# Performance work log

Measured on AMD Instinct MI355X. Metric: run time of the kernel, lower is better.

The kernel has to match this reference:

```python
import jax, jax.numpy as jnp
import numpy as np

N, E, D, H, K = 8192, 8, 1024, 4096, 2


def setup_inputs() -> dict:
    key = jax.random.key(0)
    ks = jax.random.split(key, 12)
    s = 0.02  # init scale for weights
    return {
        "x": jax.random.normal(ks[0], (N, D), jnp.float32),
        "noise": jax.random.normal(ks[1], (N, E), jnp.float32),
        "Wg_w": jax.random.normal(ks[2], (D, E), jnp.float32) * s,
        "Wg_b": jnp.zeros((E,), jnp.float32),
        "Wn_w": jax.random.normal(ks[3], (D, E), jnp.float32) * s,
        "Wn_b": jnp.zeros((E,), jnp.float32),
        "w1": jax.random.normal(ks[4], (E, D, H), jnp.float32) * s,
        "b1": jnp.zeros((E, H), jnp.float32),
        "w2": jax.random.normal(ks[5], (E, H, D), jnp.float32) * s,
        "b2": jnp.zeros((E, D), jnp.float32),
        "k": K,
    }


def reference(x, noise, Wg_w, Wg_b, Wn_w, Wn_b, w1, b1, w2, b2, k):
    # --- noisy top-k gating: H(x) = Wg(x) + noise * softplus(Wn(x)) ---
    g_logits = x @ Wg_w + Wg_b                       # [N, E]
    n_scale = jax.nn.softplus(x @ Wn_w + Wn_b)       # [N, E]
    h = g_logits + noise * n_scale                   # [N, E]
    topk_vals, topk_inds = jax.lax.top_k(h, k)       # [N, k]
    gates = jax.nn.softmax(topk_vals, axis=-1)       # [N, k]

    # Scatter top-k gates into a dense [N, E] map (zeros for unselected experts),
    # so the weighted combine is exactly sum_j gates[n,j] * expert_{inds[n,j]}(x_n).
    n_tok, n_exp = h.shape
    dense_gates = jnp.zeros((n_tok, n_exp), h.dtype).at[
        jnp.arange(n_tok)[:, None], topk_inds
    ].set(gates)                                     # [N, E]

    # --- per-expert 2-layer MLP: fc2(relu(fc1(x))) ---
    hid = jax.nn.relu(jnp.einsum('nd,edh->neh', x, w1) + b1)  # [N, E, H]
    y = jnp.einsum('neh,ehd->ned', hid, w2) + b2              # [N, E, D]
    out = jnp.einsum('ned,ne->nd', y, dense_gates)            # [N, D]
    return out
```

## Files before the change

### kernel.cpp

```cpp
#include <hip/hip_runtime.h>
#include <hip/hip_bf16.h>

#define NTOK 8192
#define NEXP 8
#define DMODEL 1024
#define DHID 4096

typedef __bf16 bf16x8 __attribute__((ext_vector_type(8)));
typedef float f32x4 __attribute__((ext_vector_type(4)));

__device__ __forceinline__ unsigned short f2bf(float f) {
  return __builtin_bit_cast(unsigned short, __float2bfloat16(f));
}

__device__ __forceinline__ void gload_lds16(const void* g, void* l) {
  __builtin_amdgcn_global_load_lds(
      (const __attribute__((address_space(1))) unsigned int*)g,
      (__attribute__((address_space(3))) unsigned int*)l, 16, 0, 0);
}

__device__ __forceinline__ int imin(int a, int b) { return a < b ? a : b; }

constexpr size_t OFF_XB   = 0;
constexpr size_t OFF_W1T  = OFF_XB + (size_t)NTOK * DMODEL * 2;
constexpr size_t OFF_W2T  = OFF_W1T + (size_t)NEXP * DHID * DMODEL * 2;
constexpr size_t OFF_HID  = OFF_W2T + (size_t)NEXP * DMODEL * DHID * 2;
constexpr size_t OFF_IDX  = OFF_HID + (size_t)NTOK * 2 * DHID * 2;
constexpr size_t OFF_GATE = OFF_IDX + (size_t)NTOK * 2 * 4;
constexpr size_t OFF_LIST = OFF_GATE + (size_t)NTOK * 2 * 4;
constexpr size_t OFF_CNT  = OFF_LIST + (size_t)NTOK * 2 * 4;
constexpr size_t OFF_OFFS = OFF_CNT + 128;
constexpr size_t OFF_CUR  = OFF_OFFS + 128;

__global__ __launch_bounds__(256) void prep_kernel(
    const float* __restrict__ w1, unsigned short* __restrict__ w1t,
    const float* __restrict__ x, const float* __restrict__ noise,
    const float* __restrict__ Wg_w, const float* __restrict__ Wg_b,
    const float* __restrict__ Wn_w, const float* __restrict__ Wn_b,
    unsigned short* __restrict__ xb, int* __restrict__ topk_idx,
    float* __restrict__ topk_gate, int* __restrict__ counts) {
  __shared__ float sh[64][65];
  const int bid = blockIdx.x;

  if (bid < 8192) {
    int e = bid >> 10, rem = bid & 1023;
    const int R = DMODEL, C = DHID;
    const float* in = w1 + (size_t)e * R * C;
    unsigned short* outp = w1t + (size_t)e * R * C;
    int r0 = (rem >> 6) * 64;
    int c0 = (rem & 63) * 64;
    int tx = threadIdx.x & 15, ty = threadIdx.x >> 4;
#pragma unroll
    for (int p = 0; p < 4; ++p) {
      int row = ty + p * 16;
      float4 v = *(const float4*)&in[(size_t)(r0 + row) * C + c0 + tx * 4];
      sh[row][tx * 4 + 0] = v.x;
      sh[row][tx * 4 + 1] = v.y;
      sh[row][tx * 4 + 2] = v.z;
      sh[row][tx * 4 + 3] = v.w;
    }
    __syncthreads();
#pragma unroll
    for (int p = 0; p < 4; ++p) {
      int crow = ty + p * 16;
      ushort4 o;
      o.x = f2bf(sh[tx * 4 + 0][crow]);
      o.y = f2bf(sh[tx * 4 + 1][crow]);
      o.z = f2bf(sh[tx * 4 + 2][crow]);
      o.w = f2bf(sh[tx * 4 + 3][crow]);
      *(ushort4*)&outp[(size_t)(c0 + crow) * R + r0 + tx * 4] = o;
    }
    return;
  }

  int g = bid - 8192;
  int wave = threadIdx.x >> 6;
  int lane = threadIdx.x & 63;
  int n = g * 4 + wave;
  if (n >= NTOK) return;

  float ag[8] = {0.f, 0.f, 0.f, 0.f, 0.f, 0.f, 0.f, 0.f};
  float an[8] = {0.f, 0.f, 0.f, 0.f, 0.f, 0.f, 0.f, 0.f};
  const float* xr = x + (size_t)n * DMODEL;
  unsigned short* xbr = xb + (size_t)n * DMODEL;
#pragma unroll 4
  for (int i = 0; i < DMODEL / 64; ++i) {
    int d = lane + i * 64;
    float xv = xr[d];
    xbr[d] = f2bf(xv);
    const float4* wg = (const float4*)(Wg_w + (size_t)d * 8);
    const float4* wn = (const float4*)(Wn_w + (size_t)d * 8);
    float4 g0 = wg[0], g1 = wg[1];
    float4 n0 = wn[0], n1 = wn[1];
    ag[0] += xv * g0.x; ag[1] += xv * g0.y; ag[2] += xv * g0.z; ag[3] += xv * g0.w;
    ag[4] += xv * g1.x; ag[5] += xv * g1.y; ag[6] += xv * g1.z; ag[7] += xv * g1.w;
    an[0] += xv * n0.x; an[1] += xv * n0.y; an[2] += xv * n0.z; an[3] += xv * n0.w;
    an[4] += xv * n1.x; an[5] += xv * n1.y; an[6] += xv * n1.z; an[7] += xv * n1.w;
  }
#pragma unroll
  for (int off = 32; off > 0; off >>= 1) {
#pragma unroll
    for (int j = 0; j < 8; ++j) {
      ag[j] += __shfl_down(ag[j], off, 64);
      an[j] += __shfl_down(an[j], off, 64);
    }
  }
  if (lane == 0) {
    float h[8];
#pragma unroll
    for (int e = 0; e < 8; ++e) {
      float gl = ag[e] + Wg_b[e];
      float z = an[e] + Wn_b[e];
      float sp = fmaxf(z, 0.f) + log1pf(expf(-fabsf(z)));
      h[e] = gl + noise[(size_t)n * 8 + e] * sp;
    }
    int i0 = 0; float v0 = h[0];
#pragma unroll
    for (int e = 1; e < 8; ++e)
      if (h[e] > v0) { v0 = h[e]; i0 = e; }
    int i1 = -1; float v1 = -1e30f;
#pragma unroll
    for (int e = 0; e < 8; ++e)
      if (e != i0 && h[e] > v1) { v1 = h[e]; i1 = e; }
    float e1 = expf(v1 - v0);
    float inv = 1.f / (1.f + e1);
    topk_idx[n * 2] = i0;
    topk_idx[n * 2 + 1] = i1;
    topk_gate[n * 2] = inv;
    topk_gate[n * 2 + 1] = e1 * inv;
    atomicAdd(&counts[i0], 1);
    atomicAdd(&counts[i1], 1);
  }
}

__global__ void scan_kernel(const int* __restrict__ counts,
                            int* __restrict__ offsets, int* __restrict__ cursor) {
  if (threadIdx.x == 0) {
    int acc = 0;
    for (int e = 0; e < NEXP; ++e) {
      offsets[e] = acc;
      cursor[e] = acc;
      acc += counts[e];
    }
    offsets[NEXP] = acc;
  }
}

__global__ void scatter_kernel(const int* __restrict__ topk_idx,
                               int* __restrict__ cursor, int* __restrict__ list) {
  int n = blockIdx.x * 256 + threadIdx.x;
  if (n >= NTOK) return;
#pragma unroll
  for (int j = 0; j < 2; ++j) {
    int e = topk_idx[n * 2 + j];
    int pos = atomicAdd(&cursor[e], 1);
    list[pos] = n * 2 + j;
  }
}

#define VMW(N) asm volatile("s_waitcnt vmcnt(" #N ")" ::: "memory")

template <int MODE>
__global__ __launch_bounds__(256, 4) void expert_gemm(
    const unsigned short* __restrict__ Asrc, const unsigned short* __restrict__ Bt,
    const float* __restrict__ bias, const int* __restrict__ offsets,
    const int* __restrict__ list, const float* __restrict__ gates,
    unsigned short* __restrict__ hid, float* __restrict__ out,
    const float* __restrict__ w2src, unsigned short* __restrict__ w2dst) {
  constexpr int Krow = MODE ? DHID : DMODEL;
  constexpr int Nout = MODE ? DMODEL : DHID;
  constexpr int NT = Krow / 32;

  __shared__ alignas(16) unsigned short Al[3][128 * 32];
  __shared__ alignas(16) unsigned short Bl[3][128 * 32];

  const int gx = gridDim.x, gy = gridDim.y;
  const int lin = blockIdx.x + gx * (blockIdx.y + gy * blockIdx.z);

  if (MODE == 0 && lin >= 16384) {
    float (*sh)[65] = reinterpret_cast<float(*)[65]>(&Al[0][0]);
    int t = lin - 16384;
    int e = t >> 10, rem = t & 1023;
    const int R = DHID, C = DMODEL;
    const float* in = w2src + (size_t)e * R * C;
    unsigned short* outp = w2dst + (size_t)e * R * C;
    int r0 = (rem >> 4) * 64;
    int c0 = (rem & 15) * 64;
    int tx = threadIdx.x & 15, ty = threadIdx.x >> 4;
#pragma unroll
    for (int p = 0; p < 4; ++p) {
      int row = ty + p * 16;
      float4 v = *(const float4*)&in[(size_t)(r0 + row) * C + c0 + tx * 4];
      sh[row][tx * 4 + 0] = v.x;
      sh[row][tx * 4 + 1] = v.y;
      sh[row][tx * 4 + 2] = v.z;
      sh[row][tx * 4 + 3] = v.w;
    }
    __syncthreads();
#pragma unroll
    for (int p = 0; p < 4; ++p) {
      int crow = ty + p * 16;
      ushort4 o;
      o.x = f2bf(sh[tx * 4 + 0][crow]);
      o.y = f2bf(sh[tx * 4 + 1][crow]);
      o.z = f2bf(sh[tx * 4 + 2][crow]);
      o.w = f2bf(sh[tx * 4 + 3][crow]);
      *(ushort4*)&outp[(size_t)(c0 + crow) * R + r0 + tx * 4] = o;
    }
    return;
  }

  const int e = lin & 7;
  int r = lin >> 3;

  int by, bx;
  if (MODE == 0) {
    int st = r >> 6;
    int inner = r & 63;
    int sm = st >> 2, sn = st & 3;
    if (sm & 1) sn = 3 - sn;
    by = sm * 8 + (inner >> 3);
    bx = sn * 8 + (inner & 7);
  } else {
    by = r & 63;
    bx = r >> 6;
  }

  const int off = offsets[e];
  const int ne = offsets[e + 1] - off;
  const int m0 = by * 128;
  if (m0 >= ne) return;
  const int n0 = bx * 128;

  const int tid = threadIdx.x;
  const int lane = tid & 63;
  const int w = tid >> 6;
  const int wm = (w >> 1) * 64;
  const int wn = (w & 1) * 64;
  const int lr = lane & 15;
  const int kg = lane >> 4;
  const int chrd = (kg ^ ((lr >> 1) & 3)) * 8;

  const unsigned short* srcA[2];
  const unsigned short* srcB[2];
#pragma unroll
  for (int i = 0; i < 2; ++i) {
    int q = tid + i * 256;
    int rr = q >> 2, c = q & 3;
    int cs = c ^ ((rr >> 1) & 3);
    int p = off + imin(m0 + rr, ne - 1);
    if (MODE == 0) {
      int token = list[p] >> 1;
      srcA[i] = Asrc + (size_t)token * DMODEL + cs * 8;
    } else {
      srcA[i] = Asrc + (size_t)p * DHID + cs * 8;
    }
    srcB[i] = Bt + (size_t)e * Nout * Krow + (size_t)(n0 + rr) * Krow + cs * 8;
  }

  f32x4 acc[4][4] = {};

  auto stage = [&](int slot, int kt) {
#pragma unroll
    for (int i = 0; i < 2; ++i) {
      int q = tid + i * 256;
      gload_lds16(srcA[i] + kt * 32, &Al[slot][q * 8]);
      gload_lds16(srcB[i] + kt * 32, &Bl[slot][q * 8]);
    }
  };

  auto compute = [&](int slot) {
    bf16x8 af[4], bfr[4];
#pragma unroll
    for (int mf = 0; mf < 4; ++mf)
      af[mf] = *(const bf16x8*)&Al[slot][(wm + mf * 16 + lr) * 32 + chrd];
#pragma unroll
    for (int nf = 0; nf < 4; ++nf)
      bfr[nf] = *(const bf16x8*)&Bl[slot][(wn + nf * 16 + lr) * 32 + chrd];
    asm volatile("s_waitcnt lgkmcnt(0)" ::: "memory");
    __builtin_amdgcn_sched_barrier(0);
#pragma unroll
    for (int mf = 0; mf < 4; ++mf)
#pragma unroll
      for (int nf = 0; nf < 4; ++nf)
        acc[mf][nf] = __builtin_amdgcn_mfma_f32_16x16x32_bf16(af[mf], bfr[nf],
                                                              acc[mf][nf], 0, 0, 0);
  };

  stage(0, 0);
  stage(1, 1);
  stage(2, 2);

  int cur = 0;
  for (int t = 0; t < NT; ++t) {
    if (t < NT - 2) { VMW(8); }
    else if (t == NT - 2) { VMW(4); }
    else { VMW(0); }
    __builtin_amdgcn_s_barrier();
    __builtin_amdgcn_sched_barrier(0);
    compute(cur);
    asm volatile("s_waitcnt lgkmcnt(0)" ::: "memory");
    __builtin_amdgcn_sched_barrier(0);
    __builtin_amdgcn_s_barrier();
    if (t + 3 < NT) stage(cur, t + 3);
    cur = (cur == 2) ? 0 : cur + 1;
  }

  if (MODE == 0) {
#pragma unroll
    for (int mf = 0; mf < 4; ++mf) {
#pragma unroll
      for (int j = 0; j < 4; ++j) {
        int rloc = wm + mf * 16 + kg * 4 + j;
        int row = m0 + rloc;
        if (row < ne) {
          size_t p = (size_t)(off + row);
#pragma unroll
          for (int nf = 0; nf < 4; ++nf) {
            int col = n0 + wn + nf * 16 + lr;
            float v = acc[mf][nf][j] + bias[(size_t)e * Nout + col];
            hid[p * DHID + col] = f2bf(fmaxf(v, 0.f));
          }
        }
      }
    }
  } else {
#pragma unroll
    for (int mf = 0; mf < 4; ++mf) {
#pragma unroll
      for (int j = 0; j < 4; ++j) {
        int rloc = wm + mf * 16 + kg * 4 + j;
        int row = m0 + rloc;
        if (row < ne) {
          int lv = list[off + row];
          int token = lv >> 1;
          float g = gates[lv];
#pragma unroll
          for (int nf = 0; nf < 4; ++nf) {
            int col = n0 + wn + nf * 16 + lr;
            float v = (acc[mf][nf][j] + bias[(size_t)e * Nout + col]) * g;
            atomicAdd(&out[(size_t)token * DMODEL + col], v);
          }
        }
      }
    }
  }
}

extern "C" void kernel_launch(void* const* d_in, const int* in_sizes, int n_in,
                              void* d_out, int out_size, void* d_ws, size_t ws_size,
                              hipStream_t stream) {
  const float* x = (const float*)d_in[0];
  const float* noise = (const float*)d_in[1];
  const float* Wg_w = (const float*)d_in[2];
  const float* Wg_b = (const float*)d_in[3];
  const float* Wn_w = (const float*)d_in[4];
  const float* Wn_b = (const float*)d_in[5];
  const float* w1 = (const float*)d_in[6];
  const float* b1 = (const float*)d_in[7];
  const float* w2 = (const float*)d_in[8];
  const float* b2 = (const float*)d_in[9];
  float* out = (float*)d_out;

  char* ws = (char*)d_ws;
  unsigned short* xb = (unsigned short*)(ws + OFF_XB);
  unsigned short* w1t = (unsigned short*)(ws + OFF_W1T);
  unsigned short* w2t = (unsigned short*)(ws + OFF_W2T);
  unsigned short* hid = (unsigned short*)(ws + OFF_HID);
  int* topk_idx = (int*)(ws + OFF_IDX);
  float* topk_gate = (float*)(ws + OFF_GATE);
  int* list = (int*)(ws + OFF_LIST);
  int* counts = (int*)(ws + OFF_CNT);
  int* offsets = (int*)(ws + OFF_OFFS);
  int* cursor = (int*)(ws + OFF_CUR);

  hipMemsetAsync(out, 0, (size_t)NTOK * DMODEL * sizeof(float), stream);
  hipMemsetAsync(counts, 0, NEXP * sizeof(int), stream);

  prep_kernel<<<10240, 256, 0, stream>>>(w1, w1t, x, noise, Wg_w, Wg_b,
                                         Wn_w, Wn_b, xb, topk_idx, topk_gate,
                                         counts);
  scan_kernel<<<1, 64, 0, stream>>>(counts, offsets, cursor);
  scatter_kernel<<<NTOK / 256, 256, 0, stream>>>(topk_idx, cursor, list);

  expert_gemm<0><<<dim3(24576, 1, 1), 256, 0, stream>>>(
      xb, w1t, b1, offsets, list, topk_gate, hid, nullptr, w2, w2t);
  expert_gemm<1><<<dim3(8, 64, NEXP), 256, 0, stream>>>(
      hid, w2t, b2, offsets, list, topk_gate, nullptr, out, nullptr, nullptr);
}
```

Measured before the change: 813.2 us.

## Use 192x128 GEMM tiles with double buffering and fuse output zeroing into prep

Expert GEMM tiles grow from 128x128 to 192x128 (each wave computes 96x64). The LDS pipeline drops from triple to double buffering so the larger A tile fits. The block-index mapping becomes a simple 43-row-tile grid, replacing the swizzled raster, and occupancy drops to 2 blocks per CU. The hipMemset of the output is replaced by extra zeroing blocks inside prep_kernel. This cuts B-tile reloads and per-launch overhead, at the cost of a shallower prefetch pipeline, lower occupancy, possible padded-tile waste on uneven expert counts, and loss of the L2-friendly swizzle.

```diff
diff --git a/kernel.cpp b/kernel.cpp
--- a/kernel.cpp
+++ b/kernel.cpp
@@ -38,9 +38,19 @@
     const float* __restrict__ Wg_w, const float* __restrict__ Wg_b,
     const float* __restrict__ Wn_w, const float* __restrict__ Wn_b,
     unsigned short* __restrict__ xb, int* __restrict__ topk_idx,
-    float* __restrict__ topk_gate, int* __restrict__ counts) {
+    float* __restrict__ topk_gate, int* __restrict__ counts,
+    float* __restrict__ outz) {
   __shared__ float sh[64][65];
   const int bid = blockIdx.x;
+
+  if (bid >= 10240) {
+    size_t base = (size_t)(bid - 10240) * 4096 + threadIdx.x * 4;
+    float4 z = {0.f, 0.f, 0.f, 0.f};
+#pragma unroll
+    for (int i = 0; i < 4; ++i)
+      *(float4*)&outz[base + (size_t)i * 1024] = z;
+    return;
+  }
 
   if (bid < 8192) {
     int e = bid >> 10, rem = bid & 1023;
@@ -161,7 +171,7 @@
 #define VMW(N) asm volatile("s_waitcnt vmcnt(" #N ")" ::: "memory")
 
 template <int MODE>
-__global__ __launch_bounds__(256, 4) void expert_gemm(
+__global__ __launch_bounds__(256, 2) void expert_gemm(
     const unsigned short* __restrict__ Asrc, const unsigned short* __restrict__ Bt,
     const float* __restrict__ bias, const int* __restrict__ offsets,
     const int* __restrict__ list, const float* __restrict__ gates,
@@ -170,16 +180,16 @@
   constexpr int Krow = MODE ? DHID : DMODEL;
   constexpr int Nout = MODE ? DMODEL : DHID;
   constexpr int NT = Krow / 32;
-
-  __shared__ alignas(16) unsigned short Al[3][128 * 32];
-  __shared__ alignas(16) unsigned short Bl[3][128 * 32];
-
-  const int gx = gridDim.x, gy = gridDim.y;
-  const int lin = blockIdx.x + gx * (blockIdx.y + gy * blockIdx.z);
-
-  if (MODE == 0 && lin >= 16384) {
+  constexpr int GY = 43;
+
+  __shared__ alignas(16) unsigned short Al[2][192 * 32];
+  __shared__ alignas(16) unsigned short Bl[2][128 * 32];
+
+  const int lin = blockIdx.x;
+
+  if (MODE == 0 && lin >= 11008) {
     float (*sh)[65] = reinterpret_cast<float(*)[65]>(&Al[0][0]);
-    int t = lin - 16384;
+    int t = lin - 11008;
     int e = t >> 10, rem = t & 1023;
     const int R = DHID, C = DMODEL;
     const float* in = w2src + (size_t)e * R * C;
@@ -211,40 +221,29 @@
   }
 
   const int e = lin & 7;
-  int r = lin >> 3;
-
-  int by, bx;
-  if (MODE == 0) {
-    int st = r >> 6;
-    int inner = r & 63;
-    int sm = st >> 2, sn = st & 3;
-    if (sm & 1) sn = 3 - sn;
-    by = sm * 8 + (inner >> 3);
-    bx = sn * 8 + (inner & 7);
-  } else {
-    by = r & 63;
-    bx = r >> 6;
-  }
+  const int r = lin >> 3;
+  const int by = r % GY;
+  const int bx = r / GY;
 
   const int off = offsets[e];
   const int ne = offsets[e + 1] - off;
-  const int m0 = by * 128;
+  const int m0 = by * 192;
   if (m0 >= ne) return;
   const int n0 = bx * 128;
 
   const int tid = threadIdx.x;
   const int lane = tid & 63;
   const int w = tid >> 6;
-  const int wm = (w >> 1) * 64;
+  const int wm = (w >> 1) * 96;
   const int wn = (w & 1) * 64;
   const int lr = lane & 15;
   const int kg = lane >> 4;
   const int chrd = (kg ^ ((lr >> 1) & 3)) * 8;
 
-  const unsigned short* srcA[2];
+  const unsigned short* srcA[3];
   const unsigned short* srcB[2];
 #pragma unroll
-  for (int i = 0; i < 2; ++i) {
+  for (int i = 0; i < 3; ++i) {
     int q = tid + i * 256;
     int rr = q >> 2, c = q & 3;
     int cs = c ^ ((rr >> 1) & 3);
@@ -255,24 +254,30 @@
     } else {
       srcA[i] = Asrc + (size_t)p * DHID + cs * 8;
     }
+  }
+#pragma unroll
+  for (int i = 0; i < 2; ++i) {
+    int q = tid + i * 256;
+    int rr = q >> 2, c = q & 3;
+    int cs = c ^ ((rr >> 1) & 3);
     srcB[i] = Bt + (size_t)e * Nout * Krow + (size_t)(n0 + rr) * Krow + cs * 8;
   }
 
-  f32x4 acc[4][4] = {};
+  f32x4 acc[6][4] = {};
 
   auto stage = [&](int slot, int kt) {
 #pragma unroll
-    for (int i = 0; i < 2; ++i) {
-      int q = tid + i * 256;
-      gload_lds16(srcA[i] + kt * 32, &Al[slot][q * 8]);
-      gload_lds16(srcB[i] + kt * 32, &Bl[slot][q * 8]);
-    }
+    for (int i = 0; i < 3; ++i)
+      gload_lds16(srcA[i] + kt * 32, &Al[slot][(tid + i * 256) * 8]);
+#pragma unroll
+    for (int i = 0; i < 2; ++i)
+      gload_lds16(srcB[i] + kt * 32, &Bl[slot][(tid + i * 256) * 8]);
   };
 
   auto compute = [&](int slot) {
-    bf16x8 af[4], bfr[4];
-#pragma unroll
-    for (int mf = 0; mf < 4; ++mf)
+    bf16x8 af[6], bfr[4];
+#pragma unroll
+    for (int mf = 0; mf < 6; ++mf)
       af[mf] = *(const bf16x8*)&Al[slot][(wm + mf * 16 + lr) * 32 + chrd];
 #pragma unroll
     for (int nf = 0; nf < 4; ++nf)
@@ -280,7 +285,7 @@
     asm volatile("s_waitcnt lgkmcnt(0)" ::: "memory");
     __builtin_amdgcn_sched_barrier(0);
 #pragma unroll
-    for (int mf = 0; mf < 4; ++mf)
+    for (int mf = 0; mf < 6; ++mf)
 #pragma unroll
       for (int nf = 0; nf < 4; ++nf)
         acc[mf][nf] = __builtin_amdgcn_mfma_f32_16x16x32_bf16(af[mf], bfr[nf],
@@ -289,12 +294,10 @@
 
   stage(0, 0);
   stage(1, 1);
-  stage(2, 2);
 
   int cur = 0;
   for (int t = 0; t < NT; ++t) {
-    if (t < NT - 2) { VMW(8); }
-    else if (t == NT - 2) { VMW(4); }
+    if (t < NT - 1) { VMW(5); }
     else { VMW(0); }
     __builtin_amdgcn_s_barrier();
     __builtin_amdgcn_sched_barrier(0);
@@ -302,13 +305,13 @@
     asm volatile("s_waitcnt lgkmcnt(0)" ::: "memory");
     __builtin_amdgcn_sched_barrier(0);
     __builtin_amdgcn_s_barrier();
-    if (t + 3 < NT) stage(cur, t + 3);
-    cur = (cur == 2) ? 0 : cur + 1;
+    if (t + 2 < NT) stage(cur, t + 2);
+    cur ^= 1;
   }
 
   if (MODE == 0) {
 #pragma unroll
-    for (int mf = 0; mf < 4; ++mf) {
+    for (int mf = 0; mf < 6; ++mf) {
 #pragma unroll
       for (int j = 0; j < 4; ++j) {
         int rloc = wm + mf * 16 + kg * 4 + j;
@@ -326,7 +329,7 @@
     }
   } else {
 #pragma unroll
-    for (int mf = 0; mf < 4; ++mf) {
+    for (int mf = 0; mf < 6; ++mf) {
 #pragma unroll
       for (int j = 0; j < 4; ++j) {
         int rloc = wm + mf * 16 + kg * 4 + j;
@@ -374,17 +377,16 @@
   int* offsets = (int*)(ws + OFF_OFFS);
   int* cursor = (int*)(ws + OFF_CUR);
 
-  hipMemsetAsync(out, 0, (size_t)NTOK * DMODEL * sizeof(float), stream);
   hipMemsetAsync(counts, 0, NEXP * sizeof(int), stream);
 
-  prep_kernel<<<10240, 256, 0, stream>>>(w1, w1t, x, noise, Wg_w, Wg_b,
+  prep_kernel<<<12288, 256, 0, stream>>>(w1, w1t, x, noise, Wg_w, Wg_b,
                                          Wn_w, Wn_b, xb, topk_idx, topk_gate,
-                                         counts);
+                                         counts, out);
   scan_kernel<<<1, 64, 0, stream>>>(counts, offsets, cursor);
   scatter_kernel<<<NTOK / 256, 256, 0, stream>>>(topk_idx, cursor, list);
 
-  expert_gemm<0><<<dim3(24576, 1, 1), 256, 0, stream>>>(
+  expert_gemm<0><<<dim3(19200, 1, 1), 256, 0, stream>>>(
       xb, w1t, b1, offsets, list, topk_gate, hid, nullptr, w2, w2t);
-  expert_gemm<1><<<dim3(8, 64, NEXP), 256, 0, stream>>>(
+  expert_gemm<1><<<dim3(2752, 1, 1), 256, 0, stream>>>(
       hid, w2t, b2, offsets, list, topk_gate, nullptr, out, nullptr, nullptr);
 }
```

Measured after the change: 870.1 us. +7.0%, slower.
